# Optimization experiments

Hardware: AMD Instinct MI355X
Metric: run time of the kernel (lower is better)

Reference implementation:

```python
import jax, jax.numpy as jnp
import numpy as np
from jax import lax

N, K, FEAT, HID = 50000, 16, 64, 128


def _linear(x, w, b=None):
    y = x @ w.T
    return y + b if b is not None else y


def _lstm_aggr(dense, wih, whh, bih, bhh):
    # dense: [N, K, F]; torch-style LSTM, return hidden state at last timestep
    n = dense.shape[0]
    hdim = whh.shape[1]
    h0 = jnp.zeros((n, hdim), dense.dtype)

    def step(carry, xt):
        h, c = carry
        gates = xt @ wih.T + bih + h @ whh.T + bhh
        i, f, g, o = jnp.split(gates, 4, axis=-1)
        c = jax.nn.sigmoid(f) * c + jax.nn.sigmoid(i) * jnp.tanh(g)
        h = jax.nn.sigmoid(o) * jnp.tanh(c)
        return (h, c), None

    (h, _), _ = lax.scan(step, (h0, h0), jnp.swapaxes(dense, 0, 1))
    return h


def _sage(x, src, dst, max_deg, pw, pb, wih, whh, bih, bhh, llw, llb, lrw):
    # PyG SAGEConv(aggr='lstm', project=True): project+relu source feats,
    # gather messages, pad per-dst neighbor sequences, LSTM-aggregate,
    # then lin_l(aggr) + lin_r(x_root). dst must be sorted (it is, by construction).
    n = x.shape[0]
    xp = jax.nn.relu(_linear(x, pw, pb))
    msgs = xp[src]                                      # [E, F]
    e = src.shape[0]
    counts = jax.ops.segment_sum(jnp.ones((e,), jnp.int32), dst, num_segments=n)
    offsets = jnp.concatenate([jnp.zeros((1,), jnp.int32), jnp.cumsum(counts)[:-1]])
    pos = jnp.arange(e, dtype=jnp.int32) - offsets[dst]  # slot within neighborhood
    dense = jnp.zeros((n, max_deg, xp.shape[1]), xp.dtype).at[dst, pos].set(msgs)
    aggr = _lstm_aggr(dense, wih, whh, bih, bhh)
    return _linear(aggr, llw, llb) + _linear(x, lrw)


def setup_inputs() -> dict:
    key = jax.random.key(0)
    ks = jax.random.split(key, 16)
    s = 0.05
    dst = jnp.repeat(jnp.arange(N, dtype=jnp.int32), K)  # sorted by destination, fixed degree K
    src = jax.random.randint(ks[0], (N * K,), 0, N, dtype=jnp.int32)
    return {
        "x": jax.random.normal(ks[1], (N, FEAT), jnp.float32),
        "edge_index": jnp.stack([src, dst]),
        "max_deg": K,
        "p1_proj_w": jax.random.normal(ks[2], (FEAT, FEAT)) * s,
        "p1_proj_b": jnp.zeros((FEAT,)),
        "p1_wih": jax.random.normal(ks[3], (4 * FEAT, FEAT)) * s,
        "p1_whh": jax.random.normal(ks[4], (4 * FEAT, FEAT)) * s,
        "p1_bih": jnp.zeros((4 * FEAT,)),
        "p1_bhh": jnp.zeros((4 * FEAT,)),
        "p1_ll_w": jax.random.normal(ks[5], (HID // 2, FEAT)) * s,
        "p1_ll_b": jnp.zeros((HID // 2,)),
        "p1_lr_w": jax.random.normal(ks[6], (HID // 2, FEAT)) * s,
        "p2_proj_w": jax.random.normal(ks[7], (HID // 2, HID // 2)) * s,
        "p2_proj_b": jnp.zeros((HID // 2,)),
        "p2_wih": jax.random.normal(ks[8], (4 * (HID // 2), HID // 2)) * s,
        "p2_whh": jax.random.normal(ks[9], (4 * (HID // 2), HID // 2)) * s,
        "p2_bih": jnp.zeros((4 * (HID // 2),)),
        "p2_bhh": jnp.zeros((4 * (HID // 2),)),
        "p2_ll_w": jax.random.normal(ks[10], (HID, HID // 2)) * s,
        "p2_ll_b": jnp.zeros((HID,)),
        "p2_lr_w": jax.random.normal(ks[11], (HID, HID // 2)) * s,
        "lin1_w": jax.random.normal(ks[12], (HID * 3 // 2, HID)) * s,
        "lin1_b": jnp.zeros((HID * 3 // 2,)),
        "lin2_w": jax.random.normal(ks[13], (HID // 2, HID * 3 // 2)) * s,
        "lin2_b": jnp.zeros((HID // 2,)),
        "lin3_w": jax.random.normal(ks[14], (HID // 2, HID // 2)) * s,
        "lin3_b": jnp.zeros((HID // 2,)),
    }


def reference(x, edge_index, max_deg,
              p1_proj_w, p1_proj_b, p1_wih, p1_whh, p1_bih, p1_bhh, p1_ll_w, p1_ll_b, p1_lr_w,
              p2_proj_w, p2_proj_b, p2_wih, p2_whh, p2_bih, p2_bhh, p2_ll_w, p2_ll_b, p2_lr_w,
              lin1_w, lin1_b, lin2_w, lin2_b, lin3_w, lin3_b):
    src, dst = edge_index[0], edge_index[1]
    h = jax.nn.relu(_sage(x, src, dst, max_deg, p1_proj_w, p1_proj_b, p1_wih, p1_whh, p1_bih, p1_bhh, p1_ll_w, p1_ll_b, p1_lr_w))
    h = jax.nn.relu(_sage(h, src, dst, max_deg, p2_proj_w, p2_proj_b, p2_wih, p2_whh, p2_bih, p2_bhh, p2_ll_w, p2_ll_b, p2_lr_w))
    h = jax.nn.relu(_linear(h, lin1_w, lin1_b))
    h = jax.nn.relu(_linear(h, lin2_w, lin2_b))
    h = jax.nn.relu(_linear(h, lin3_w, lin3_b))
    return (h, edge_index)
```

## Files before the change

### kernel.cpp

```cpp
#include <hip/hip_runtime.h>
#include <hip/hip_bf16.h>

typedef unsigned short u16;
typedef unsigned int u32;
typedef __attribute__((ext_vector_type(8))) short short8;
typedef __attribute__((ext_vector_type(4))) float f32x4;

#define KS1 1.44269504f
#define KS2 2.88539008f

__device__ __forceinline__ float bf2f(u16 u) {
    union { u32 i; float f; } v; v.i = ((u32)u) << 16; return v.f;
}
__device__ __forceinline__ u16 f2bf(float f) {
    union { float f; u32 i; } v; v.f = f;
    u32 r = v.i + 0x7fffu + ((v.i >> 16) & 1u);
    return (u16)(r >> 16);
}
__device__ __forceinline__ u32 pack_bf2(float lo, float hi) {
    return __builtin_amdgcn_perm(__float_as_uint(hi), __float_as_uint(lo), 0x07060302u);
}
__device__ __forceinline__ u32 pack_relu(float a, float b) {
    return (u32)f2bf(fmaxf(a, 0.f)) | ((u32)f2bf(fmaxf(b, 0.f)) << 16);
}
__device__ __forceinline__ f32x4 bias4(const u16* b) {
    uint2 u = *(const uint2*)b;
    f32x4 r;
    r[0] = bf2f((u16)(u.x & 0xffffu)); r[1] = bf2f((u16)(u.x >> 16));
    r[2] = bf2f((u16)(u.y & 0xffffu)); r[3] = bf2f((u16)(u.y >> 16));
    return r;
}
__device__ __forceinline__ void barrier_lds() {
    asm volatile("s_waitcnt lgkmcnt(0)" ::: "memory");
    __builtin_amdgcn_s_barrier();
}
__device__ __forceinline__ void xwrite(u16* buf, int D2, int row, int quad, int jt, u32 w0, u32 w1) {
    int ch = jt * 2 + (quad >> 1);
    *(uint2*)(buf + row * D2 + ((ch ^ (row & 7)) << 3) + ((quad & 1) << 2)) = (uint2){w0, w1};
}
__device__ __forceinline__ short8 xread(const u16* buf, int D2, int row, int quad, int kc) {
    return *(const short8*)(buf + row * D2 + (((kc * 4 + quad) ^ (row & 7)) << 3));
}
#define MFMA16 __builtin_amdgcn_mfma_f32_16x16x32_bf16

__global__ __launch_bounds__(256) void k_pre(
    const u16* __restrict__ X, const u16* __restrict__ pw, const u16* __restrict__ pb,
    u16* __restrict__ XP, int M, int gb,
    const int* __restrict__ e, float* __restrict__ eout, int n4, int eb,
    const u16* __restrict__ w1i, const u16* __restrict__ w1h,
    const u16* __restrict__ w2i, const u16* __restrict__ w2h,
    u16* __restrict__ wss)
{
    const int bid = blockIdx.x;
    const int tid = threadIdx.x;
    if (bid >= gb + eb) {
        int wb = bid - gb - eb;
        int mi = wb >> 4;
        const u16* Wsrc = (mi == 0) ? w1i : (mi == 1) ? w1h : (mi == 2) ? w2i : w2h;
        u16* Wdst = wss + (size_t)mi * 16384;
        int e0 = (wb & 15) * 1024 + tid * 4;
        int row = e0 >> 6;
        float sc = (row >= 128 && row < 192) ? KS2 : KS1;
        uint2 v = *(const uint2*)(Wsrc + e0);
        u32 a = (u32)f2bf(bf2f((u16)(v.x & 0xffffu)) * sc)
              | ((u32)f2bf(bf2f((u16)(v.x >> 16)) * sc) << 16);
        u32 b = (u32)f2bf(bf2f((u16)(v.y & 0xffffu)) * sc)
              | ((u32)f2bf(bf2f((u16)(v.y >> 16)) * sc) << 16);
        *(uint2*)(Wdst + e0) = (uint2){a, b};
        return;
    }
    if (bid >= gb) {
        int i = (bid - gb) * 256 + tid;
        if (i < n4) {
            int4 v = *(const int4*)(e + (size_t)i * 4);
            float4 o;
            o.x = (float)v.x; o.y = (float)v.y; o.z = (float)v.z; o.w = (float)v.w;
            *(float4*)(eout + (size_t)i * 4) = o;
        }
        return;
    }
    const int lane = tid & 63;
    const int wave = tid >> 6;
    const int row0 = (bid * 4 + wave) * 16;
    if (row0 >= M) return;
    const int col  = lane & 15;
    const int quad = lane >> 4;

    f32x4 c1[4];
#pragma unroll
    for (int jt = 0; jt < 4; ++jt) c1[jt] = (f32x4){0.f, 0.f, 0.f, 0.f};
    {
        const u16* xrow = X  + (size_t)(row0 + col) * 64 + quad * 8;
        const u16* wrow = pw + (size_t)col * 64 + quad * 8;
#pragma unroll
        for (int kc = 0; kc < 64; kc += 32) {
            short8 a = *(const short8*)(xrow + kc);
#pragma unroll
            for (int jt = 0; jt < 4; ++jt) {
                short8 b = *(const short8*)(wrow + (size_t)jt * 16 * 64 + kc);
                c1[jt] = MFMA16(a, b, c1[jt], 0, 0, 0);
            }
        }
    }
#pragma unroll
    for (int jt = 0; jt < 4; ++jt) {
        float bias = bf2f(pb[jt * 16 + col]);
#pragma unroll
        for (int r = 0; r < 4; ++r) {
            float v = fmaxf(c1[jt][r] + bias, 0.f);
            XP[(size_t)(row0 + quad * 4 + r) * 64 + jt * 16 + col] = f2bf(v);
        }
    }
}


#define NONLIN(ACC, CST, HW0, HW1)                                             \
    {                                                                          \
        float hv[4];                                                           \
        _Pragma("unroll") for (int r = 0; r < 4; ++r) {                        \
            float iv = ACC[0][r], fv = ACC[1][r], gv = ACC[2][r], ov = ACC[3][r]; \
            float e_i = __builtin_amdgcn_exp2f(-iv);                           \
            float e_f = __builtin_amdgcn_exp2f(-fv);                           \
            float e_g = __builtin_amdgcn_exp2f(gv);                            \
            float af  = 1.0f + e_f;                                            \
            float P   = (1.0f + e_i) * (1.0f + e_g);                           \
            float tt  = __builtin_fmaf(e_g, KS2, -KS2);                        \
            float num = __builtin_fmaf(tt, af, CST[r] * P);                    \
            float cn  = num * __builtin_amdgcn_rcpf(af * P);                   \
            CST[r] = cn;                                                       \
            float e_c = __builtin_amdgcn_exp2f(cn);                            \
            float e_o = __builtin_amdgcn_exp2f(-ov);                           \
            float roc = __builtin_amdgcn_rcpf((1.0f + e_o) * (1.0f + e_c));    \
            hv[r] = (e_c - 1.0f) * roc;                                        \
        }                                                                      \
        HW0 = pack_bf2(hv[0], hv[1]);                                          \
        HW1 = pack_bf2(hv[2], hv[3]);                                          \
    }

#define LSTM2S_PROLOGUE                                                        \
    const int tid  = threadIdx.x;                                              \
    const int lane = tid & 63;                                                 \
    const int w    = tid >> 6;                                                 \
    const int col  = lane & 15;                                                \
    const int quad = lane >> 4;                                                \
    const int node0 = blockIdx.x * 32;                                         \
    if (node0 >= N) return;                                                    \
    const bool actB = (node0 + 32 <= N);                                       \
    const int nodeA = node0 + col;                                             \
    const int nodeB = actB ? (node0 + 16 + col) : nodeA;                       \
    {                                                                          \
        int j = tid;                                                           \
        float sc = (j >= 128 && j < 192) ? KS2 : KS1;                          \
        lds_b[j] = (bf2f(bih[j]) + bf2f(bhh[j])) * sc;                         \
    }                                                                          \
    const int sr  = tid >> 3;                           \
    const int sch = tid & 7;                            \
    const int srow = (node0 + sr < N) ? (node0 + sr) : (N - 1);                \
    const int* sbase = src + (size_t)srow * 16;                               \
    const u16* gsb = xp + (size_t)sch * 8;                                     \
    u16* sdst = xs + sr * 64 + ((sch ^ (sr & 7)) << 3);                        \
    short8 sg[4];                                                              \
    {                                                                          \
        int4 sv = *(const int4*)(sbase);                                       \
        short8 a0 = *(const short8*)(gsb + (size_t)sv.x * 64);                 \
        short8 a1 = *(const short8*)(gsb + (size_t)sv.y * 64);                 \
        short8 a2 = *(const short8*)(gsb + (size_t)sv.z * 64);                 \
        short8 a3 = *(const short8*)(gsb + (size_t)sv.w * 64);                 \
        *(short8*)(sdst + 0)    = a0;                                          \
        *(short8*)(sdst + 2048) = a1;                                          \
        *(short8*)(sdst + 4096) = a2;                                          \
        *(short8*)(sdst + 6144) = a3;                                          \
        sv = *(const int4*)(sbase + 4);                                        \
        sg[0] = *(const short8*)(gsb + (size_t)sv.x * 64);                     \
        sg[1] = *(const short8*)(gsb + (size_t)sv.y * 64);                     \
        sg[2] = *(const short8*)(gsb + (size_t)sv.z * 64);                     \
        sg[3] = *(const short8*)(gsb + (size_t)sv.w * 64);                     \
    }                                                                          \
    short8 wf[8], hf[8];                                                       \
    _Pragma("unroll") for (int g = 0; g < 4; ++g) {                            \
        int jt = w + 4 * g;                                                    \
        const u16* wi = wihs + (size_t)(jt * 16 + col) * 64 + quad * 8;        \
        const u16* wh = whhs + (size_t)(jt * 16 + col) * 64 + quad * 8;        \
        wf[g * 2 + 0] = *(const short8*)(wi);                                  \
        wf[g * 2 + 1] = *(const short8*)(wi + 32);                             \
        hf[g * 2 + 0] = *(const short8*)(wh);                                  \
        hf[g * 2 + 1] = *(const short8*)(wh + 32);                             \
    }                                                                          \
    __syncthreads();                                                           \
    const int q0 = quad ^ (col & 7);                                           \
    short8 xbA0, xbA1, xbB0, xbB1;                                             \
    {                                                                          \
        const u16* pA = xs + col * 64;                                         \
        xbA0 = *(const short8*)(pA + q0 * 8);                                  \
        xbA1 = *(const short8*)(pA + ((q0 ^ 4) << 3));                         \
        const u16* pB = pA + 1024;                                             \
        xbB0 = *(const short8*)(pB + q0 * 8);                                  \
        xbB1 = *(const short8*)(pB + ((q0 ^ 4) << 3));                         \
    }

#define LSTM2S_CORE_LOOP                                                       \
    short8 z8 = (short8){0,0,0,0,0,0,0,0};                                     \
    short8 hbA0 = z8, hbA1 = z8, hbB0 = z8, hbB1 = z8;                         \
    float cA[4], cB[4];                                                        \
    _Pragma("unroll") for (int i = 0; i < 4; ++i) { cA[i] = 0.f; cB[i] = 0.f; }\
    _Pragma("unroll 1") for (int t = 0; t < 16; ++t) {                         \
        u16* hbuf = lds_h[t & 1];                                              \
        f32x4 accA[4], accB[4];                                                \
        _Pragma("unroll") for (int g = 0; g < 4; ++g) {                        \
            f32x4 bc = *(const f32x4*)(lds_b + (w + 4 * g) * 16 + quad * 4);   \
            accA[g] = MFMA16(wf[g * 2 + 0], xbA0, bc, 0, 0, 0);                \
            accB[g] = MFMA16(wf[g * 2 + 0], xbB0, bc, 0, 0, 0);                \
            accA[g] = MFMA16(wf[g * 2 + 1], xbA1, accA[g], 0, 0, 0);           \
            accB[g] = MFMA16(wf[g * 2 + 1], xbB1, accB[g], 0, 0, 0);           \
        }                                                                      \
        if (t > 0) {                                                           \
            _Pragma("unroll") for (int g = 0; g < 4; ++g) {                    \
                accA[g] = MFMA16(hf[g * 2 + 0], hbA0, accA[g], 0, 0, 0);       \
                accB[g] = MFMA16(hf[g * 2 + 0], hbB0, accB[g], 0, 0, 0);       \
                accA[g] = MFMA16(hf[g * 2 + 1], hbA1, accA[g], 0, 0, 0);       \
                accB[g] = MFMA16(hf[g * 2 + 1], hbB1, accB[g], 0, 0, 0);       \
            }                                                                  \
        }                                                                      \
        u32 hwA0, hwA1, hwB0, hwB1;                                            \
        NONLIN(accA, cA, hwA0, hwA1)                                           \
        NONLIN(accB, cB, hwB0, hwB1)                                           \
        xwrite(hbuf, 64, col,      quad, w, hwA0, hwA1);                       \
        xwrite(hbuf, 64, col + 16, quad, w, hwB0, hwB1);                       \
        barrier_lds();                                                         \
        if ((t & 3) == 3 && t < 15) {                                          \
            *(short8*)(sdst + 0)    = sg[0];                                   \
            *(short8*)(sdst + 2048) = sg[1];                                   \
            *(short8*)(sdst + 4096) = sg[2];                                   \
            *(short8*)(sdst + 6144) = sg[3];                                   \
            barrier_lds();                                                     \
            if (t <= 7) {                                                      \
                int4 sv = *(const int4*)(sbase + (t >> 2) * 4 + 8);            \
                sg[0] = *(const short8*)(gsb + (size_t)sv.x * 64);             \
                sg[1] = *(const short8*)(gsb + (size_t)sv.y * 64);             \
                sg[2] = *(const short8*)(gsb + (size_t)sv.z * 64);             \
                sg[3] = *(const short8*)(gsb + (size_t)sv.w * 64);             \
            }                                                                  \
        }                                                                      \
        hbA0 = xread(hbuf, 64, col,      quad, 0);                             \
        hbA1 = xread(hbuf, 64, col,      quad, 1);                             \
        hbB0 = xread(hbuf, 64, col + 16, quad, 0);                             \
        hbB1 = xread(hbuf, 64, col + 16, quad, 1);                             \
        if (t < 15) {                                                          \
            const u16* pA = xs + ((t + 1) & 3) * 2048 + col * 64;              \
            xbA0 = *(const short8*)(pA + q0 * 8);                              \
            xbA1 = *(const short8*)(pA + ((q0 ^ 4) << 3));                     \
            const u16* pB = pA + 1024;                                         \
            xbB0 = *(const short8*)(pB + q0 * 8);                              \
            xbB1 = *(const short8*)(pB + ((q0 ^ 4) << 3));                     \
        }                                                                      \
    }

__global__ __launch_bounds__(256, 3) void lstm_mid(
    const u16* __restrict__ xp, const int* __restrict__ src,
    const u16* __restrict__ wihs, const u16* __restrict__ whhs,
    const u16* __restrict__ bih, const u16* __restrict__ bhh,
    const u16* __restrict__ X,
    const u16* __restrict__ llw, const u16* __restrict__ llb,
    const u16* __restrict__ lrw,
    const u16* __restrict__ pw, const u16* __restrict__ pb,
    u16* __restrict__ Y1, u16* __restrict__ XP2, int N)
{
    __shared__ u16 xs[4 * 2048];
    __shared__ float lds_b[256];
    __shared__ u16 lds_h[2][32 * 64];
    u16* bufY = xs;

    LSTM2S_PROLOGUE
    LSTM2S_CORE_LOOP

    {
        const u16* wr  = llw + (size_t)(w * 16 + col) * 64 + quad * 8;
        short8 ll0 = *(const short8*)wr, ll1 = *(const short8*)(wr + 32);
        const u16* wr2 = lrw + (size_t)(w * 16 + col) * 64 + quad * 8;
        short8 lr0 = *(const short8*)wr2, lr1 = *(const short8*)(wr2 + 32);
        f32x4 bY = bias4(llb + w * 16 + quad * 4);

        const u16* xrA = X + (size_t)nodeA * 64 + quad * 8;
        short8 rxA0 = *(const short8*)xrA, rxA1 = *(const short8*)(xrA + 32);
        const u16* xrB = X + (size_t)nodeB * 64 + quad * 8;
        short8 rxB0 = *(const short8*)xrB, rxB1 = *(const short8*)(xrB + 32);

        f32x4 aA = MFMA16(ll0, hbA0, bY, 0, 0, 0);
        aA = MFMA16(ll1, hbA1, aA, 0, 0, 0);
        aA = MFMA16(lr0, rxA0, aA, 0, 0, 0);
        aA = MFMA16(lr1, rxA1, aA, 0, 0, 0);
        f32x4 aB = MFMA16(ll0, hbB0, bY, 0, 0, 0);
        aB = MFMA16(ll1, hbB1, aB, 0, 0, 0);
        aB = MFMA16(lr0, rxB0, aB, 0, 0, 0);
        aB = MFMA16(lr1, rxB1, aB, 0, 0, 0);

        u32 yA0 = pack_relu(aA[0], aA[1]), yA1 = pack_relu(aA[2], aA[3]);
        u32 yB0 = pack_relu(aB[0], aB[1]), yB1 = pack_relu(aB[2], aB[3]);
        *(uint2*)(Y1 + (size_t)nodeA * 64 + w * 16 + quad * 4) = (uint2){yA0, yA1};
        if (actB) *(uint2*)(Y1 + (size_t)nodeB * 64 + w * 16 + quad * 4) = (uint2){yB0, yB1};
        xwrite(bufY, 64, col,      quad, w, yA0, yA1);
        xwrite(bufY, 64, col + 16, quad, w, yB0, yB1);
        __syncthreads();

        const u16* wp = pw + (size_t)(w * 16 + col) * 64 + quad * 8;
        short8 p0 = *(const short8*)wp, p1 = *(const short8*)(wp + 32);
        f32x4 bp = bias4(pb + w * 16 + quad * 4);

        short8 ybA0 = xread(bufY, 64, col,      quad, 0);
        short8 ybA1 = xread(bufY, 64, col,      quad, 1);
        short8 ybB0 = xread(bufY, 64, col + 16, quad, 0);
        short8 ybB1 = xread(bufY, 64, col + 16, quad, 1);

        f32x4 a2A = MFMA16(p0, ybA0, bp, 0, 0, 0);
        a2A = MFMA16(p1, ybA1, a2A, 0, 0, 0);
        f32x4 a2B = MFMA16(p0, ybB0, bp, 0, 0, 0);
        a2B = MFMA16(p1, ybB1, a2B, 0, 0, 0);

        *(uint2*)(XP2 + (size_t)nodeA * 64 + w * 16 + quad * 4) =
            (uint2){pack_relu(a2A[0], a2A[1]), pack_relu(a2A[2], a2A[3])};
        if (actB) *(uint2*)(XP2 + (size_t)nodeB * 64 + w * 16 + quad * 4) =
            (uint2){pack_relu(a2B[0], a2B[1]), pack_relu(a2B[2], a2B[3])};
    }
}

__global__ __launch_bounds__(256, 3) void lstm_post(
    const u16* __restrict__ xp, const int* __restrict__ src,
    const u16* __restrict__ wihs, const u16* __restrict__ whhs,
    const u16* __restrict__ bih, const u16* __restrict__ bhh,
    const u16* __restrict__ Y1,
    const u16* __restrict__ llw2, const u16* __restrict__ llb2,
    const u16* __restrict__ lrw2,
    const u16* __restrict__ w1m, const u16* __restrict__ b1m,
    const u16* __restrict__ w2m, const u16* __restrict__ b2m,
    const u16* __restrict__ w3m, const u16* __restrict__ b3m,
    float* __restrict__ outp, int N)
{
    __shared__ u16 xs[4 * 2048];
    __shared__ float lds_b[256];
    __shared__ u16 lds_h[2][32 * 64];
    u16* bufA = (u16*)lds_h;
    u16* bufB = xs;

    LSTM2S_PROLOGUE
    LSTM2S_CORE_LOOP

    {
        barrier_lds();

        const u16* yrA = Y1 + (size_t)nodeA * 64 + quad * 8;
        short8 ryA0 = *(const short8*)yrA, ryA1 = *(const short8*)(yrA + 32);
        const u16* yrB = Y1 + (size_t)nodeB * 64 + quad * 8;
        short8 ryB0 = *(const short8*)yrB, ryB1 = *(const short8*)(yrB + 32);

#pragma unroll
        for (int ti = 0; ti < 2; ++ti) {
            int jt = 2 * w + ti;
            const u16* wr = llw2 + (size_t)(jt * 16 + col) * 64 + quad * 8;
            short8 l0 = *(const short8*)wr, l1 = *(const short8*)(wr + 32);
            const u16* wr2 = lrw2 + (size_t)(jt * 16 + col) * 64 + quad * 8;
            short8 r0 = *(const short8*)wr2, r1 = *(const short8*)(wr2 + 32);
            f32x4 b0 = bias4(llb2 + jt * 16 + quad * 4);
            f32x4 aA = MFMA16(l0, hbA0, b0, 0, 0, 0);
            aA = MFMA16(l1, hbA1, aA, 0, 0, 0);
            aA = MFMA16(r0, ryA0, aA, 0, 0, 0);
            aA = MFMA16(r1, ryA1, aA, 0, 0, 0);
            xwrite(bufA, 128, col, quad, jt, pack_relu(aA[0], aA[1]), pack_relu(aA[2], aA[3]));
            f32x4 aB = MFMA16(l0, hbB0, b0, 0, 0, 0);
            aB = MFMA16(l1, hbB1, aB, 0, 0, 0);
            aB = MFMA16(r0, ryB0, aB, 0, 0, 0);
            aB = MFMA16(r1, ryB1, aB, 0, 0, 0);
            xwrite(bufA, 128, col + 16, quad, jt, pack_relu(aB[0], aB[1]), pack_relu(aB[2], aB[3]));
        }
        __syncthreads();

        short8 y2A[4], y2B[4];
#pragma unroll
        for (int kc = 0; kc < 4; ++kc) {
            y2A[kc] = xread(bufA, 128, col,      quad, kc);
            y2B[kc] = xread(bufA, 128, col + 16, quad, kc);
        }
#pragma unroll
        for (int ti = 0; ti < 3; ++ti) {
            int jt = 3 * w + ti;
            const u16* wr = w1m + (size_t)(jt * 16 + col) * 128 + quad * 8;
            short8 wk[4];
#pragma unroll
            for (int kc = 0; kc < 4; ++kc) wk[kc] = *(const short8*)(wr + kc * 32);
            f32x4 b1v = bias4(b1m + jt * 16 + quad * 4);
            f32x4 aA = b1v, aB = b1v;
#pragma unroll
            for (int kc = 0; kc < 4; ++kc) {
                aA = MFMA16(wk[kc], y2A[kc], aA, 0, 0, 0);
                aB = MFMA16(wk[kc], y2B[kc], aB, 0, 0, 0);
            }
            xwrite(bufB, 192, col,      quad, jt, pack_relu(aA[0], aA[1]), pack_relu(aA[2], aA[3]));
            xwrite(bufB, 192, col + 16, quad, jt, pack_relu(aB[0], aB[1]), pack_relu(aB[2], aB[3]));
        }
        __syncthreads();

        short8 t1A[6], t1B[6];
#pragma unroll
        for (int kc = 0; kc < 6; ++kc) {
            t1A[kc] = xread(bufB, 192, col,      quad, kc);
            t1B[kc] = xread(bufB, 192, col + 16, quad, kc);
        }
        {
            const u16* wr = w2m + (size_t)(w * 16 + col) * 192 + quad * 8;
            f32x4 b2v = bias4(b2m + w * 16 + quad * 4);
            f32x4 aA = b2v, aB = b2v;
#pragma unroll
            for (int kc = 0; kc < 6; ++kc) {
                short8 wk = *(const short8*)(wr + kc * 32);
                aA = MFMA16(wk, t1A[kc], aA, 0, 0, 0);
                aB = MFMA16(wk, t1B[kc], aB, 0, 0, 0);
            }
            xwrite(bufA, 64, col,      quad, w, pack_relu(aA[0], aA[1]), pack_relu(aA[2], aA[3]));
            xwrite(bufA, 64, col + 16, quad, w, pack_relu(aB[0], aB[1]), pack_relu(aB[2], aB[3]));
        }
        __syncthreads();

        short8 t2A0 = xread(bufA, 64, col,      quad, 0);
        short8 t2A1 = xread(bufA, 64, col,      quad, 1);
        short8 t2B0 = xread(bufA, 64, col + 16, quad, 0);
        short8 t2B1 = xread(bufA, 64, col + 16, quad, 1);
        {
            const u16* wr = w3m + (size_t)(w * 16 + col) * 64 + quad * 8;
            short8 l0 = *(const short8*)wr, l1 = *(const short8*)(wr + 32);
            f32x4 b3v = bias4(b3m + w * 16 + quad * 4);
            f32x4 aA = MFMA16(l0, t2A0, b3v, 0, 0, 0);
            aA = MFMA16(l1, t2A1, aA, 0, 0, 0);
            f32x4 aB = MFMA16(l0, t2B0, b3v, 0, 0, 0);
            aB = MFMA16(l1, t2B1, aB, 0, 0, 0);
            float4 oA;
            oA.x = fmaxf(aA[0], 0.f); oA.y = fmaxf(aA[1], 0.f);
            oA.z = fmaxf(aA[2], 0.f); oA.w = fmaxf(aA[3], 0.f);
            *(float4*)(outp + (size_t)nodeA * 64 + w * 16 + quad * 4) = oA;
            if (actB) {
                float4 oB;
                oB.x = fmaxf(aB[0], 0.f); oB.y = fmaxf(aB[1], 0.f);
                oB.z = fmaxf(aB[2], 0.f); oB.w = fmaxf(aB[3], 0.f);
                *(float4*)(outp + (size_t)nodeB * 64 + w * 16 + quad * 4) = oB;
            }
        }
    }
}

extern "C" void kernel_launch(void* const* d_in, const int* in_sizes, int n_in,
                              void* d_out, int out_size, void* d_ws, size_t ws_size,
                              hipStream_t stream)
{
    const u16* x       = (const u16*)d_in[0];
    const int* edge    = (const int*)d_in[1];
    const u16* p1_pw   = (const u16*)d_in[3];
    const u16* p1_pb   = (const u16*)d_in[4];
    const u16* p1_wih  = (const u16*)d_in[5];
    const u16* p1_whh  = (const u16*)d_in[6];
    const u16* p1_bih  = (const u16*)d_in[7];
    const u16* p1_bhh  = (const u16*)d_in[8];
    const u16* p1_llw  = (const u16*)d_in[9];
    const u16* p1_llb  = (const u16*)d_in[10];
    const u16* p1_lrw  = (const u16*)d_in[11];
    const u16* p2_pw   = (const u16*)d_in[12];
    const u16* p2_pb   = (const u16*)d_in[13];
    const u16* p2_wih  = (const u16*)d_in[14];
    const u16* p2_whh  = (const u16*)d_in[15];
    const u16* p2_bih  = (const u16*)d_in[16];
    const u16* p2_bhh  = (const u16*)d_in[17];
    const u16* p2_llw  = (const u16*)d_in[18];
    const u16* p2_llb  = (const u16*)d_in[19];
    const u16* p2_lrw  = (const u16*)d_in[20];
    const u16* lin1w   = (const u16*)d_in[21];
    const u16* lin1b   = (const u16*)d_in[22];
    const u16* lin2w   = (const u16*)d_in[23];
    const u16* lin2b   = (const u16*)d_in[24];
    const u16* lin3w   = (const u16*)d_in[25];
    const u16* lin3b   = (const u16*)d_in[26];
    (void)n_in; (void)ws_size;

    const int N  = in_sizes[0] / 64;
    const int E2 = in_sizes[1];
    const int* srcIdx = edge;

    char* w = (char*)d_ws;
    u16* wss   = (u16*)(w);
    u16* xp1   = (u16*)(w + 1u  * 1024 * 1024);
    u16* xp2   = (u16*)(w + 8u  * 1024 * 1024);
    u16* bufY1 = (u16*)(w + 15u * 1024 * 1024);
    u16* wih1s = wss;
    u16* whh1s = wss + 16384;
    u16* wih2s = wss + 32768;
    u16* whh2s = wss + 49152;

    float* out_h    = (float*)d_out;
    float* out_edge = (float*)d_out + (size_t)N * 64;
    (void)out_size;

    const int gb  = (N + 63) / 64;
    const int gbl = (N + 31) / 32;
    const int n4 = E2 / 4;
    const int eb = (n4 + 255) / 256;

    dim3 block(256);

    hipLaunchKernelGGL(k_pre, dim3(gb + eb + 64), block, 0, stream,
                       x, p1_pw, p1_pb, xp1, N, gb,
                       edge, out_edge, n4, eb,
                       p1_wih, p1_whh, p2_wih, p2_whh, wss);
    hipLaunchKernelGGL(lstm_mid, dim3(gbl), block, 0, stream,
                       xp1, srcIdx, wih1s, whh1s, p1_bih, p1_bhh,
                       x, p1_llw, p1_llb, p1_lrw, p2_pw, p2_pb, bufY1, xp2, N);
    hipLaunchKernelGGL(lstm_post, dim3(gbl), block, 0, stream,
                       xp2, srcIdx, wih2s, whh2s, p2_bih, p2_bhh,
                       bufY1, p2_llw, p2_llb, p2_lrw,
                       lin1w, lin1b, lin2w, lin2b, lin3w, lin3b, out_h, N);
}
```

Measured before the change: 295.1 us.

## Gather LSTM neighbor messages directly into LDS with async global_load_lds

Replaces the register-staged gather of neighbor messages (load to VGPRs, then write to LDS with an extra barrier every four steps) with direct global-to-LDS loads issued in the prologue and at steps 4 and 8. LDS staging doubles to eight timestep slots so two groups of four steps are in flight, and the per-step input fragments are now read from LDS at the top of each step. Explicit vmcnt waits before steps 7 and 11 replace the extra barriers. This frees registers and removes barriers, at the cost of more LDS per block (possible occupancy loss) and reliance on vmcnt waits for cross-wave visibility, which may be fragile without a barrier.

```diff
diff --git a/kernel.cpp b/kernel.cpp
--- a/kernel.cpp
+++ b/kernel.cpp
@@ -33,6 +33,11 @@
 __device__ __forceinline__ void barrier_lds() {
     asm volatile("s_waitcnt lgkmcnt(0)" ::: "memory");
     __builtin_amdgcn_s_barrier();
+}
+__device__ __forceinline__ void gload_lds16(const u16* g, u16* l) {
+    __builtin_amdgcn_global_load_lds(
+        (const __attribute__((address_space(1))) u32*)(const void*)g,
+        (__attribute__((address_space(3))) u32*)(void*)l, 16, 0, 0);
 }
 __device__ __forceinline__ void xwrite(u16* buf, int D2, int row, int quad, int jt, u32 w0, u32 w1) {
     int ch = jt * 2 + (quad >> 1);
@@ -137,7 +142,7 @@
         HW1 = pack_bf2(hv[2], hv[3]);                                          \
     }
 
-#define LSTM2S_PROLOGUE                                                        \
+#define LSTM2G_PROLOGUE                                                        \
     const int tid  = threadIdx.x;                                              \
     const int lane = tid & 63;                                                 \
     const int w    = tid >> 6;                                                 \
@@ -153,28 +158,16 @@
         float sc = (j >= 128 && j < 192) ? KS2 : KS1;                          \
         lds_b[j] = (bf2f(bih[j]) + bf2f(bhh[j])) * sc;                         \
     }                                                                          \
-    const int sr  = tid >> 3;                           \
-    const int sch = tid & 7;                            \
-    const int srow = (node0 + sr < N) ? (node0 + sr) : (N - 1);                \
-    const int* sbase = src + (size_t)srow * 16;                               \
-    const u16* gsb = xp + (size_t)sch * 8;                                     \
-    u16* sdst = xs + sr * 64 + ((sch ^ (sr & 7)) << 3);                        \
-    short8 sg[4];                                                              \
-    {                                                                          \
-        int4 sv = *(const int4*)(sbase);                                       \
-        short8 a0 = *(const short8*)(gsb + (size_t)sv.x * 64);                 \
-        short8 a1 = *(const short8*)(gsb + (size_t)sv.y * 64);                 \
-        short8 a2 = *(const short8*)(gsb + (size_t)sv.z * 64);                 \
-        short8 a3 = *(const short8*)(gsb + (size_t)sv.w * 64);                 \
-        *(short8*)(sdst + 0)    = a0;                                          \
-        *(short8*)(sdst + 2048) = a1;                                          \
-        *(short8*)(sdst + 4096) = a2;                                          \
-        *(short8*)(sdst + 6144) = a3;                                          \
-        sv = *(const int4*)(sbase + 4);                                        \
-        sg[0] = *(const short8*)(gsb + (size_t)sv.x * 64);                     \
-        sg[1] = *(const short8*)(gsb + (size_t)sv.y * 64);                     \
-        sg[2] = *(const short8*)(gsb + (size_t)sv.z * 64);                     \
-        sg[3] = *(const short8*)(gsb + (size_t)sv.w * 64);                     \
+    const int rlo = lane >> 3;                               \
+    const u16* gch = xp + (((lane & 7) ^ rlo) << 3);   \
+    int i2k[4], i3k[4];                                                        \
+    _Pragma("unroll") for (int k = 0; k < 4; ++k) {                            \
+        int rn = node0 + k * 8 + rlo; if (rn >= N) rn = N - 1;                 \
+        const int* sp = src + (size_t)rn * 16;                                 \
+        int i0 = sp[w], i1 = sp[4 + w];                                        \
+        i2k[k] = sp[8 + w]; i3k[k] = sp[12 + w];                               \
+        gload_lds16(gch + (size_t)i0 * 64, xs + w * 2048 + k * 512);           \
+        gload_lds16(gch + (size_t)i1 * 64, xs + (4 + w) * 2048 + k * 512);     \
     }                                                                          \
     short8 wf[8], hf[8];                                                       \
     _Pragma("unroll") for (int g = 0; g < 4; ++g) {                            \
@@ -187,24 +180,31 @@
         hf[g * 2 + 1] = *(const short8*)(wh + 32);                             \
     }                                                                          \
     __syncthreads();                                                           \
-    const int q0 = quad ^ (col & 7);                                           \
-    short8 xbA0, xbA1, xbB0, xbB1;                                             \
-    {                                                                          \
-        const u16* pA = xs + col * 64;                                         \
-        xbA0 = *(const short8*)(pA + q0 * 8);                                  \
-        xbA1 = *(const short8*)(pA + ((q0 ^ 4) << 3));                         \
-        const u16* pB = pA + 1024;                                             \
-        xbB0 = *(const short8*)(pB + q0 * 8);                                  \
-        xbB1 = *(const short8*)(pB + ((q0 ^ 4) << 3));                         \
-    }
-
-#define LSTM2S_CORE_LOOP                                                       \
+    const int q0 = quad ^ (col & 7);
+
+#define LSTM2G_CORE_LOOP                                                       \
     short8 z8 = (short8){0,0,0,0,0,0,0,0};                                     \
     short8 hbA0 = z8, hbA1 = z8, hbB0 = z8, hbB1 = z8;                         \
     float cA[4], cB[4];                                                        \
     _Pragma("unroll") for (int i = 0; i < 4; ++i) { cA[i] = 0.f; cB[i] = 0.f; }\
     _Pragma("unroll 1") for (int t = 0; t < 16; ++t) {                         \
-        u16* hbuf = lds_h[t & 1];                                              \
+        if (t == 7 || t == 11)                                                 \
+            asm volatile("s_waitcnt vmcnt(0)" ::: "memory");                   \
+        const u16* pS = xs + ((((t >> 2) & 1) * 4 + (t & 3)) * 2048);          \
+        const u16* pA = pS + col * 64;                                         \
+        short8 xbA0 = *(const short8*)(pA + q0 * 8);                           \
+        short8 xbA1 = *(const short8*)(pA + ((q0 ^ 4) << 3));                  \
+        const u16* pB = pS + (col + 16) * 64;                                  \
+        short8 xbB0 = *(const short8*)(pB + q0 * 8);                           \
+        short8 xbB1 = *(const short8*)(pB + ((q0 ^ 4) << 3));                  \
+        if (t == 4) {            \
+            _Pragma("unroll") for (int k = 0; k < 4; ++k)                      \
+                gload_lds16(gch + (size_t)i2k[k] * 64, xs + w * 2048 + k * 512); \
+        }                                                                      \
+        if (t == 8) {         \
+            _Pragma("unroll") for (int k = 0; k < 4; ++k)                      \
+                gload_lds16(gch + (size_t)i3k[k] * 64, xs + (4 + w) * 2048 + k * 512); \
+        }                                                                      \
         f32x4 accA[4], accB[4];                                                \
         _Pragma("unroll") for (int g = 0; g < 4; ++g) {                        \
             f32x4 bc = *(const f32x4*)(lds_b + (w + 4 * g) * 16 + quad * 4);   \
@@ -224,35 +224,14 @@
         u32 hwA0, hwA1, hwB0, hwB1;                                            \
         NONLIN(accA, cA, hwA0, hwA1)                                           \
         NONLIN(accB, cB, hwB0, hwB1)                                           \
+        u16* hbuf = lds_h[t & 1];                                              \
         xwrite(hbuf, 64, col,      quad, w, hwA0, hwA1);                       \
         xwrite(hbuf, 64, col + 16, quad, w, hwB0, hwB1);                       \
         barrier_lds();                                                         \
-        if ((t & 3) == 3 && t < 15) {                                          \
-            *(short8*)(sdst + 0)    = sg[0];                                   \
-            *(short8*)(sdst + 2048) = sg[1];                                   \
-            *(short8*)(sdst + 4096) = sg[2];                                   \
-            *(short8*)(sdst + 6144) = sg[3];                                   \
-            barrier_lds();                                                     \
-            if (t <= 7) {                                                      \
-                int4 sv = *(const int4*)(sbase + (t >> 2) * 4 + 8);            \
-                sg[0] = *(const short8*)(gsb + (size_t)sv.x * 64);             \
-                sg[1] = *(const short8*)(gsb + (size_t)sv.y * 64);             \
-                sg[2] = *(const short8*)(gsb + (size_t)sv.z * 64);             \
-                sg[3] = *(const short8*)(gsb + (size_t)sv.w * 64);             \
-            }                                                                  \
-        }                                                                      \
         hbA0 = xread(hbuf, 64, col,      quad, 0);                             \
         hbA1 = xread(hbuf, 64, col,      quad, 1);                             \
         hbB0 = xread(hbuf, 64, col + 16, quad, 0);                             \
         hbB1 = xread(hbuf, 64, col + 16, quad, 1);                             \
-        if (t < 15) {                                                          \
-            const u16* pA = xs + ((t + 1) & 3) * 2048 + col * 64;              \
-            xbA0 = *(const short8*)(pA + q0 * 8);                              \
-            xbA1 = *(const short8*)(pA + ((q0 ^ 4) << 3));                     \
-            const u16* pB = pA + 1024;                                         \
-            xbB0 = *(const short8*)(pB + q0 * 8);                              \
-            xbB1 = *(const short8*)(pB + ((q0 ^ 4) << 3));                     \
-        }                                                                      \
     }
 
 __global__ __launch_bounds__(256, 3) void lstm_mid(
@@ -265,13 +244,13 @@
     const u16* __restrict__ pw, const u16* __restrict__ pb,
     u16* __restrict__ Y1, u16* __restrict__ XP2, int N)
 {
-    __shared__ u16 xs[4 * 2048];
+    __shared__ u16 xs[8 * 2048];
     __shared__ float lds_b[256];
     __shared__ u16 lds_h[2][32 * 64];
     u16* bufY = xs;
 
-    LSTM2S_PROLOGUE
-    LSTM2S_CORE_LOOP
+    LSTM2G_PROLOGUE
+    LSTM2G_CORE_LOOP
 
     {
         const u16* wr  = llw + (size_t)(w * 16 + col) * 64 + quad * 8;
@@ -335,14 +314,14 @@
     const u16* __restrict__ w3m, const u16* __restrict__ b3m,
     float* __restrict__ outp, int N)
 {
-    __shared__ u16 xs[4 * 2048];
+    __shared__ u16 xs[8 * 2048];
     __shared__ float lds_b[256];
     __shared__ u16 lds_h[2][32 * 64];
     u16* bufA = (u16*)lds_h;
     u16* bufB = xs;
 
-    LSTM2S_PROLOGUE
-    LSTM2S_CORE_LOOP
+    LSTM2G_PROLOGUE
+    LSTM2G_CORE_LOOP
 
     {
         barrier_lds();
```

Result: faster. 281.0 us (-4.8%).
